# Performance work log

Measured on AMD Instinct MI355X. Metric: run time of the kernel, lower is better.

## Reference

```python
import jax, jax.numpy as jnp
import numpy as np

S1 = 2048      # seqx1_dim
S2 = 2048      # seqx2_dim
E1 = 1024      # seqx1_emb_dim
E2 = 1024      # seqx2_emb_dim
U = 1024       # units
M = E1 + E2    # margex_dim
B = 2048
TAU = 0.5


def setup_inputs() -> dict:
    key = jax.random.key(0)
    ks = jax.random.split(key, 20)
    g = lambda k, shp, fan: jax.random.normal(k, shp, jnp.float32) * (1.0 / np.sqrt(fan))
    bias = jnp.zeros((4 * U,), jnp.float32).at[U:2 * U].set(1.0)  # unit_forget_bias
    return {
        'inputs': jax.random.normal(ks[0], (B, S1 + S2), jnp.float32),
        'h_tm1': jax.random.normal(ks[1], (B, U), jnp.float32),
        'c_tm1': jax.random.normal(ks[2], (B, U), jnp.float32),
        'crohis_tm': jax.random.normal(ks[3], (B, M), jnp.float32),
        'embed_w1': g(ks[4], (S1, E1), S1),
        'embed_w2': g(ks[5], (S2, E2), S2),
        'w12_w': g(ks[6], (E1, E1), E1),
        'w12_u': g(ks[7], (E2, E1), E2),
        'w12_v': g(ks[8], (E2, E1), E2),
        'w21_w': g(ks[9], (E2, E2), E2),
        'w21_u': g(ks[10], (E1, E2), E1),
        'w21_v': g(ks[11], (E1, E2), E1),
        'crohis_w': g(ks[12], (M, U), M),
        'crohis_b': jnp.zeros((U,), jnp.float32),
        'decomp_w': g(ks[13], (M, M), M),
        'decomp_b': jnp.zeros((M,), jnp.float32),
        'kernel': g(ks[14], (M, 4 * U), M),
        'recurrent_kernel': g(ks[15], (U, 4 * U), U),
        'bias': bias,
    }


def _cell(inputs, h_tm1, c_tm1, crohis_tm, embed_w1, embed_w2, w12_w, w12_u, w12_v,
          w21_w, w21_u, w21_v, crohis_w, crohis_b, decomp_w, decomp_b,
          kernel, recurrent_kernel, bias):
    seqx1 = inputs[:, :S1]
    seqx2 = inputs[:, S1:]
    e1 = seqx1 @ embed_w1                                   # [B,E1]
    e2 = seqx2 @ embed_w2                                   # [B,E2]
    # dual cross-attention gates (softmax over feature axis, as K.softmax default)
    ca12 = jax.nn.softmax(jnp.tanh(e1 @ w12_w + e2 @ w12_u) * (e2 @ w12_v), axis=-1)
    ca21 = jax.nn.softmax(jnp.tanh(e2 @ w21_w + e1 @ w21_u) * (e1 @ w21_v), axis=-1)
    x = jnp.concatenate([e1 * ca12, e2 * ca21], axis=-1)    # [B,M]
    # cross-history decomposition gate and decayed merge
    decomp = jax.nn.sigmoid(crohis_tm @ decomp_w + decomp_b)
    crohis = TAU * crohis_tm * decomp + (1.0 - TAU) * x     # [B,M]
    h_cro = jnp.tanh(crohis @ crohis_w + crohis_b)          # [B,U]
    # fused LSTM (implementation=2)
    z = x @ kernel + h_tm1 @ recurrent_kernel + bias        # [B,4U]
    zi, zf, zc, zo = jnp.split(z, 4, axis=-1)
    i = jax.nn.sigmoid(zi)
    f = jax.nn.sigmoid(zf)
    c = f * c_tm1 + i * jnp.tanh(zc)
    o = jax.nn.sigmoid(zo)
    h = o * jnp.tanh(c) + h_cro
    return h, c, crohis


def reference(inputs, h_tm1, c_tm1, crohis_tm, embed_w1, embed_w2, w12_w, w12_u, w12_v,
              w21_w, w21_u, w21_v, crohis_w, crohis_b, decomp_w, decomp_b,
              kernel, recurrent_kernel, bias):
    return _cell(inputs, h_tm1, c_tm1, crohis_tm, embed_w1, embed_w2, w12_w, w12_u,
                 w12_v, w21_w, w21_u, w21_v, crohis_w, crohis_b, decomp_w, decomp_b,
                 kernel, recurrent_kernel, bias)
```

## Files before the change

### kernel.cpp

```cpp
#include <hip/hip_runtime.h>
#include <stdint.h>

typedef unsigned short u16;
typedef __bf16 bf16x8 __attribute__((ext_vector_type(8)));
typedef float f32x4 __attribute__((ext_vector_type(4)));
typedef u16 u16x8 __attribute__((ext_vector_type(8)));

__device__ __forceinline__ u16 bf16_bits(float f) {
  uint32_t x = __float_as_uint(f);
  uint32_t r = (x + 0x7FFFu + ((x >> 16) & 1u)) >> 16;
  return (u16)r;
}
__device__ __forceinline__ float bits_f32(u16 u) {
  return __uint_as_float(((uint32_t)u) << 16);
}
__device__ __forceinline__ float sigm(float x) { return 1.f / (1.f + expf(-x)); }

__device__ __forceinline__ void gload_lds16(const void* g, void* l) {
  __builtin_amdgcn_global_load_lds(
      (const __attribute__((address_space(1))) void*)g,
      (__attribute__((address_space(3))) void*)l,
      16, 0, 0);
}

__global__ __launch_bounds__(256) void cvt_all_kernel(
    const float* __restrict__ inp, const float* __restrict__ ctm,
    const float* __restrict__ h, u16* __restrict__ bf_in,
    u16* __restrict__ bf_ctm, u16* __restrict__ xh) {
  int i = blockIdx.x * 256 + threadIdx.x;
  const float* src;
  u16* dst;
  if (i < 1048576) {
    src = inp + (size_t)i * 8;
    dst = bf_in + (size_t)i * 8;
  } else if (i < 1048576 + 524288) {
    int j = i - 1048576;
    src = ctm + (size_t)j * 8;
    dst = bf_ctm + (size_t)j * 8;
  } else {
    int j = i - 1572864;
    int row = j >> 7;
    int c0 = (j & 127) << 3;
    src = h + (size_t)row * 1024 + c0;
    dst = xh + (size_t)row * 3072 + 2048 + c0;
  }
  const f32x4* s = (const f32x4*)src;
  f32x4 a = s[0], b = s[1];
  u16x8 o;
#pragma unroll
  for (int k = 0; k < 4; ++k) { o[k] = bf16_bits(a[k]); o[4 + k] = bf16_bits(b[k]); }
  *(u16x8*)dst = o;
}

struct TransGroups {
  const float* src[12];
  u16* dst[12];
  int N[12];
  int ld[12];
  long long off[12];
  int start[13];
};

__global__ __launch_bounds__(256) void transpose_all_kernel(TransGroups tg) {
  __shared__ float t[64][33];
  int bid = blockIdx.x;
  int g = 0;
#pragma unroll
  for (int i = 1; i < 12; ++i)
    if (bid >= tg.start[i]) g = i;
  int local = bid - tg.start[g];
  const float* src = tg.src[g];
  u16* dst = tg.dst[g];
  int N = tg.N[g];
  int ld = tg.ld[g];
  long long off = tg.off[g];
  int ntn = N >> 5;
  int n0 = (local % ntn) << 5;
  int k0 = (local / ntn) << 6;
  int tx = threadIdx.x & 31, ty = threadIdx.x >> 5;
#pragma unroll
  for (int r = ty; r < 64; r += 8) t[r][tx] = src[(size_t)(k0 + r) * N + n0 + tx];
  __syncthreads();
#pragma unroll
  for (int j = ty; j < 32; j += 8) {
    uint32_t lo = bf16_bits(t[2 * tx][j]);
    uint32_t hi = bf16_bits(t[2 * tx + 1][j]);
    *(uint32_t*)(&dst[off + (size_t)(n0 + j) * ld + k0 + 2 * tx]) = lo | (hi << 16);
  }
}

enum { EPI_F32 = 0, EPI_BF16 = 1, EPI_DHALF = 2, EPI_TANH = 3 };

struct GemmGroups {
  const u16* A[4];
  const u16* Bt[4];
  float* C[4];
  u16* Cb[4];
  const float* bias[4];
  const float* aux[4];
  int lda[4];
  int K[4];
  int nbx[4];
  int ldc[4];
  int ldcb[4];
  int epi[4];
  int start[4];
};

__global__ __launch_bounds__(256) void gemm_grouped(GemmGroups gg) {
  __shared__ u16 As[2][4096];
  __shared__ u16 Bs[2][4096];
  const int bid = blockIdx.x;
  int g = 0;
#pragma unroll
  for (int i = 1; i < 4; ++i)
    if (bid >= gg.start[i]) g = i;
  const int local = bid - gg.start[g];
  const u16* __restrict__ A = gg.A[g];
  const u16* __restrict__ Bt = gg.Bt[g];
  const int lda = gg.lda[g];
  const int K = gg.K[g];
  const int nbx = gg.nbx[g];

  const int tid = threadIdx.x;
  const int lane = tid & 63;
  const int wid = tid >> 6;
  const int wr = wid >> 1, wc = wid & 1;
  const int brow = (local / nbx) * 128;
  const int bcol = (local % nbx) * 128;

  f32x4 acc[4][4] = {};

  const int s0 = wid, s1 = wid + 4;
  const int oA0 = s0 * 1024 + lane * 16;
  const int oA1 = s1 * 1024 + lane * 16;

  const char* gA0 = (const char*)A + (((size_t)(brow + (oA0 >> 6)) * lda) << 1) + (oA0 & 63);
  const char* gA1 = (const char*)A + (((size_t)(brow + (oA1 >> 6)) * lda) << 1) + (oA1 & 63);
  const char* gB0 = (const char*)Bt + (((size_t)(bcol + (oA0 >> 6)) * K) << 1) + (oA0 & 63);
  const char* gB1 = (const char*)Bt + (((size_t)(bcol + (oA1 >> 6)) * K) << 1) + (oA1 & 63);

#define STAGE(buf, koff)                                              \
  {                                                                   \
    gload_lds16(gA0 + (koff), (char*)As + (buf) * 8192 + s0 * 1024);  \
    gload_lds16(gA1 + (koff), (char*)As + (buf) * 8192 + s1 * 1024);  \
    gload_lds16(gB0 + (koff), (char*)Bs + (buf) * 8192 + s0 * 1024);  \
    gload_lds16(gB1 + (koff), (char*)Bs + (buf) * 8192 + s1 * 1024);  \
  }

  const int nk = K >> 5;
  STAGE(0, 0);
  __syncthreads();
  int cur = 0;
  for (int kt = 0; kt < nk; ++kt) {
    const int koff = (kt + 1 < nk ? kt + 1 : kt) << 6;
    STAGE(cur ^ 1, koff);

    const char* Ab = (const char*)As + cur * 8192;
    const char* Bb = (const char*)Bs + cur * 8192;
    bf16x8 af[4], bfr[4];
#pragma unroll
    for (int m = 0; m < 4; ++m) {
      int r = wr * 64 + m * 16 + (lane & 15);
      af[m] = *(const bf16x8*)(Ab + r * 64 + ((lane >> 4) << 4));
    }
#pragma unroll
    for (int n = 0; n < 4; ++n) {
      int cidx = wc * 64 + n * 16 + (lane & 15);
      bfr[n] = *(const bf16x8*)(Bb + cidx * 64 + ((lane >> 4) << 4));
    }
#pragma unroll
    for (int m = 0; m < 4; ++m)
#pragma unroll
      for (int n = 0; n < 4; ++n)
        acc[m][n] = __builtin_amdgcn_mfma_f32_16x16x32_bf16(af[m], bfr[n], acc[m][n], 0, 0, 0);

    __syncthreads();
    cur ^= 1;
  }
#undef STAGE

  float* __restrict__ C = gg.C[g];
  u16* __restrict__ Cb = gg.Cb[g];
  const float* __restrict__ bias = gg.bias[g];
  const float* __restrict__ aux = gg.aux[g];
  const int ldc = gg.ldc[g];
  const int ldcb = gg.ldcb[g];
  const int epi = gg.epi[g];

  const int r0 = brow + wr * 64 + ((lane >> 4) << 2);
  const int c0 = bcol + wc * 64 + (lane & 15);
#pragma unroll
  for (int m = 0; m < 4; ++m) {
#pragma unroll
    for (int n = 0; n < 4; ++n) {
#pragma unroll
      for (int j = 0; j < 4; ++j) {
        int gr = r0 + m * 16 + j;
        int gc = c0 + n * 16;
        float v = acc[m][n][j];
        if (epi == EPI_F32) {
          C[(size_t)gr * ldc + gc] = v;
        } else if (epi == EPI_BF16) {
          Cb[(size_t)gr * ldcb + gc] = bf16_bits(v);
        } else if (epi == EPI_DHALF) {
          size_t ci = (size_t)gr * ldc + gc;
          C[ci] = 0.5f * aux[ci] * sigm(v + bias[gc]);
        } else {
          C[(size_t)gr * ldc + gc] = tanhf(v + bias[gc]);
        }
      }
    }
  }
}

__global__ __launch_bounds__(256) void softmax_cro_kernel(
    const float* __restrict__ T_ALL, const u16* __restrict__ E_B,
    const float* __restrict__ DCRO, u16* __restrict__ XH_B,
    float* __restrict__ out_cro, u16* __restrict__ CRO_B) {
  __shared__ float smx[4], sms[4];
  int row = blockIdx.x >> 1;
  int half = blockIdx.x & 1;
  const float* T = T_ALL + (size_t)row * 4096 + half * 1024;
  const float* V = T_ALL + (size_t)row * 4096 + 2048 + half * 1024;
  int tid = threadIdx.x;
  float s[4];
  float lmax = -1e30f;
#pragma unroll
  for (int i = 0; i < 4; ++i) {
    int c = tid + (i << 8);
    s[i] = tanhf(T[c]) * V[c];
    lmax = fmaxf(lmax, s[i]);
  }
#pragma unroll
  for (int o = 32; o; o >>= 1) lmax = fmaxf(lmax, __shfl_xor(lmax, o, 64));
  if ((tid & 63) == 0) smx[tid >> 6] = lmax;
  __syncthreads();
  float bmax = fmaxf(fmaxf(smx[0], smx[1]), fmaxf(smx[2], smx[3]));
  float lsum = 0.f;
#pragma unroll
  for (int i = 0; i < 4; ++i) { s[i] = expf(s[i] - bmax); lsum += s[i]; }
#pragma unroll
  for (int o = 32; o; o >>= 1) lsum += __shfl_xor(lsum, o, 64);
  if ((tid & 63) == 0) sms[tid >> 6] = lsum;
  __syncthreads();
  float inv = 1.f / (sms[0] + sms[1] + sms[2] + sms[3]);
#pragma unroll
  for (int i = 0; i < 4; ++i) {
    int c = tid + (i << 8);
    int col = half * 1024 + c;
    size_t mi = (size_t)row * 2048 + col;
    float x = bits_f32(E_B[mi]) * s[i] * inv;
    XH_B[(size_t)row * 3072 + col] = bf16_bits(x);
    float cro = DCRO[mi] + 0.5f * x;
    out_cro[mi] = cro;
    CRO_B[mi] = bf16_bits(cro);
  }
}

__global__ __launch_bounds__(256) void gates_kernel(
    const float* __restrict__ Z, const float* __restrict__ bias,
    const float* __restrict__ c_tm1, const float* __restrict__ hcro,
    float* __restrict__ out_h, float* __restrict__ out_c) {
  int i = blockIdx.x * 256 + threadIdx.x;
  int row = i >> 8;
  int u0 = (i & 255) << 2;
  const float* zr = Z + (size_t)row * 4096;
  f32x4 zi = *(const f32x4*)(zr + u0);
  f32x4 zf = *(const f32x4*)(zr + 1024 + u0);
  f32x4 zc = *(const f32x4*)(zr + 2048 + u0);
  f32x4 zo = *(const f32x4*)(zr + 3072 + u0);
  f32x4 bi = *(const f32x4*)(bias + u0);
  f32x4 bff = *(const f32x4*)(bias + 1024 + u0);
  f32x4 bc = *(const f32x4*)(bias + 2048 + u0);
  f32x4 bo = *(const f32x4*)(bias + 3072 + u0);
  f32x4 ct = *(const f32x4*)(c_tm1 + (size_t)row * 1024 + u0);
  f32x4 hc = *(const f32x4*)(hcro + (size_t)row * 1024 + u0);
  f32x4 h, c;
#pragma unroll
  for (int k = 0; k < 4; ++k) {
    float I = sigm(zi[k] + bi[k]);
    float F = sigm(zf[k] + bff[k]);
    float O = sigm(zo[k] + bo[k]);
    float cc = F * ct[k] + I * tanhf(zc[k] + bc[k]);
    c[k] = cc;
    h[k] = O * tanhf(cc) + hc[k];
  }
  *(f32x4*)(out_h + (size_t)row * 1024 + u0) = h;
  *(f32x4*)(out_c + (size_t)row * 1024 + u0) = c;
}

extern "C" void kernel_launch(void* const* d_in, const int* in_sizes, int n_in,
                              void* d_out, int out_size, void* d_ws, size_t ws_size,
                              hipStream_t stream) {
  const float* in_inputs = (const float*)d_in[0];
  const float* in_h      = (const float*)d_in[1];
  const float* in_c      = (const float*)d_in[2];
  const float* in_ctm    = (const float*)d_in[3];
  const float* w_e1      = (const float*)d_in[4];
  const float* w_e2      = (const float*)d_in[5];
  const float* w12w      = (const float*)d_in[6];
  const float* w12u      = (const float*)d_in[7];
  const float* w12v      = (const float*)d_in[8];
  const float* w21w      = (const float*)d_in[9];
  const float* w21u      = (const float*)d_in[10];
  const float* w21v      = (const float*)d_in[11];
  const float* w_cro     = (const float*)d_in[12];
  const float* b_cro     = (const float*)d_in[13];
  const float* w_dec     = (const float*)d_in[14];
  const float* b_dec     = (const float*)d_in[15];
  const float* w_k       = (const float*)d_in[16];
  const float* w_rk      = (const float*)d_in[17];
  const float* b_z       = (const float*)d_in[18];

  float* out_h   = (float*)d_out;
  float* out_c   = out_h + (size_t)2048 * 1024;
  float* out_cro = out_h + (size_t)2 * 2048 * 1024;

  char* ws = (char*)d_ws;
  size_t off = 0;
  auto alloc = [&](size_t bytes) {
    char* p = ws + off;
    off += (bytes + 255) & ~(size_t)255;
    return p;
  };
  u16* BF_IN    = (u16*)alloc((size_t)2048 * 4096 * 2);
  u16* BF_CROTM = (u16*)alloc((size_t)2048 * 2048 * 2);
  u16* E_B      = (u16*)alloc((size_t)2048 * 2048 * 2);
  float* T_ALL  = (float*)alloc((size_t)2048 * 4096 * 4);
  float* DCRO   = (float*)alloc((size_t)2048 * 2048 * 4);
  u16* XH_B     = (u16*)alloc((size_t)2048 * 3072 * 2);
  u16* CRO_B    = (u16*)alloc((size_t)2048 * 2048 * 2);
  float* HCRO   = (float*)alloc((size_t)2048 * 1024 * 4);
  u16* WT_E1    = (u16*)alloc((size_t)1024 * 2048 * 2);
  u16* WT_E2    = (u16*)alloc((size_t)1024 * 2048 * 2);
  u16* WT_T     = (u16*)alloc((size_t)2048 * 2048 * 2);
  u16* WT_V12   = (u16*)alloc((size_t)1024 * 1024 * 2);
  u16* WT_V21   = (u16*)alloc((size_t)1024 * 1024 * 2);
  u16* WT_CRO   = (u16*)alloc((size_t)1024 * 2048 * 2);
  u16* WT_DEC   = (u16*)alloc((size_t)2048 * 2048 * 2);
  u16* WT_KRK   = (u16*)alloc((size_t)4096 * 3072 * 2);
  float* Z = T_ALL;

  const int INF = 0x7fffffff;

  cvt_all_kernel<<<7168, 256, 0, stream>>>(in_inputs, in_ctm, in_h, BF_IN, BF_CROTM, XH_B);

  {
    TransGroups tg;
    int s = 0, gi = 0;
    auto add = [&](const float* src, int K, int N, u16* dst, int ld, long long dOff) {
      tg.src[gi] = src; tg.dst[gi] = dst; tg.N[gi] = N; tg.ld[gi] = ld; tg.off[gi] = dOff;
      tg.start[gi] = s; s += (K >> 6) * (N >> 5); ++gi;
    };
    add(w_e1, 2048, 1024, WT_E1, 2048, 0);
    add(w_e2, 2048, 1024, WT_E2, 2048, 0);
    add(w12w, 1024, 1024, WT_T, 2048, 0);
    add(w12u, 1024, 1024, WT_T, 2048, 1024);
    add(w21u, 1024, 1024, WT_T, 2048, (long long)1024 * 2048);
    add(w21w, 1024, 1024, WT_T, 2048, (long long)1024 * 2048 + 1024);
    add(w12v, 1024, 1024, WT_V12, 1024, 0);
    add(w21v, 1024, 1024, WT_V21, 1024, 0);
    add(w_cro, 2048, 1024, WT_CRO, 2048, 0);
    add(w_dec, 2048, 2048, WT_DEC, 2048, 0);
    add(w_k, 2048, 4096, WT_KRK, 3072, 0);
    add(w_rk, 1024, 4096, WT_KRK, 3072, 2048);
    tg.start[12] = s;
    transpose_all_kernel<<<s, 256, 0, stream>>>(tg);
  }

  auto mkgrp = [&]() {
    GemmGroups gg;
    for (int i = 0; i < 4; ++i) {
      gg.A[i] = nullptr; gg.Bt[i] = nullptr; gg.C[i] = nullptr; gg.Cb[i] = nullptr;
      gg.bias[i] = nullptr; gg.aux[i] = nullptr;
      gg.lda[i] = 0; gg.K[i] = 32; gg.nbx[i] = 1; gg.ldc[i] = 0; gg.ldcb[i] = 0;
      gg.epi[i] = EPI_F32; gg.start[i] = INF;
    }
    return gg;
  };

  {
    GemmGroups gg = mkgrp();
    gg.A[0] = BF_CROTM; gg.Bt[0] = WT_DEC; gg.lda[0] = 2048; gg.K[0] = 2048;
    gg.nbx[0] = 16; gg.C[0] = DCRO; gg.ldc[0] = 2048; gg.epi[0] = EPI_DHALF;
    gg.bias[0] = b_dec; gg.aux[0] = in_ctm; gg.start[0] = 0;
    gg.A[1] = BF_IN; gg.Bt[1] = WT_E1; gg.lda[1] = 4096; gg.K[1] = 2048;
    gg.nbx[1] = 8; gg.Cb[1] = E_B; gg.ldcb[1] = 2048; gg.epi[1] = EPI_BF16;
    gg.start[1] = 256;
    gg.A[2] = BF_IN + 2048; gg.Bt[2] = WT_E2; gg.lda[2] = 4096; gg.K[2] = 2048;
    gg.nbx[2] = 8; gg.Cb[2] = E_B + 1024; gg.ldcb[2] = 2048; gg.epi[2] = EPI_BF16;
    gg.start[2] = 384;
    gemm_grouped<<<512, 256, 0, stream>>>(gg);
  }

  {
    GemmGroups gg = mkgrp();
    gg.A[0] = E_B; gg.Bt[0] = WT_T; gg.lda[0] = 2048; gg.K[0] = 2048;
    gg.nbx[0] = 16; gg.C[0] = T_ALL; gg.ldc[0] = 4096; gg.epi[0] = EPI_F32;
    gg.start[0] = 0;
    gg.A[1] = E_B + 1024; gg.Bt[1] = WT_V12; gg.lda[1] = 2048; gg.K[1] = 1024;
    gg.nbx[1] = 8; gg.C[1] = T_ALL + 2048; gg.ldc[1] = 4096; gg.epi[1] = EPI_F32;
    gg.start[1] = 256;
    gg.A[2] = E_B; gg.Bt[2] = WT_V21; gg.lda[2] = 2048; gg.K[2] = 1024;
    gg.nbx[2] = 8; gg.C[2] = T_ALL + 3072; gg.ldc[2] = 4096; gg.epi[2] = EPI_F32;
    gg.start[2] = 384;
    gemm_grouped<<<512, 256, 0, stream>>>(gg);
  }

  softmax_cro_kernel<<<4096, 256, 0, stream>>>(T_ALL, E_B, DCRO, XH_B, out_cro, CRO_B);

  {
    GemmGroups gg = mkgrp();
    gg.A[0] = XH_B; gg.Bt[0] = WT_KRK; gg.lda[0] = 3072; gg.K[0] = 3072;
    gg.nbx[0] = 32; gg.C[0] = Z; gg.ldc[0] = 4096; gg.epi[0] = EPI_F32;
    gg.start[0] = 0;
    gg.A[1] = CRO_B; gg.Bt[1] = WT_CRO; gg.lda[1] = 2048; gg.K[1] = 2048;
    gg.nbx[1] = 8; gg.C[1] = HCRO; gg.ldc[1] = 1024; gg.epi[1] = EPI_TANH;
    gg.bias[1] = b_cro; gg.start[1] = 512;
    gemm_grouped<<<640, 256, 0, stream>>>(gg);
  }

  gates_kernel<<<2048, 256, 0, stream>>>(Z, b_z, in_c, HCRO, out_h, out_c);
}
```

Baseline: 497.8 us.

## Split-K GEMM groups to double block count and fold reductions into consumers

Adds a separate B leading dimension so each GEMM can be split along K into two groups writing partial sums. The two partials are combined in the softmax and gates kernels, which also take over the tanh epilogue for the cross-history projection. The V projections are now stored as bf16. The intent is to raise the number of blocks per launch (512→768, 640→1280) to fill the many CUs, at the cost of extra fp32 partial-sum traffic and reduced bf16 precision on V.

```diff
diff --git a/kernel.cpp b/kernel.cpp
--- a/kernel.cpp
+++ b/kernel.cpp
@@ -89,7 +89,7 @@
   }
 }
 
-enum { EPI_F32 = 0, EPI_BF16 = 1, EPI_DHALF = 2, EPI_TANH = 3 };
+enum { EPI_F32 = 0, EPI_BF16 = 1, EPI_DHALF = 2 };
 
 struct GemmGroups {
   const u16* A[4];
@@ -99,6 +99,7 @@
   const float* bias[4];
   const float* aux[4];
   int lda[4];
+  int ldb[4];
   int K[4];
   int nbx[4];
   int ldc[4];
@@ -119,6 +120,7 @@
   const u16* __restrict__ A = gg.A[g];
   const u16* __restrict__ Bt = gg.Bt[g];
   const int lda = gg.lda[g];
+  const int ldb = gg.ldb[g];
   const int K = gg.K[g];
   const int nbx = gg.nbx[g];
 
@@ -137,8 +139,8 @@
 
   const char* gA0 = (const char*)A + (((size_t)(brow + (oA0 >> 6)) * lda) << 1) + (oA0 & 63);
   const char* gA1 = (const char*)A + (((size_t)(brow + (oA1 >> 6)) * lda) << 1) + (oA1 & 63);
-  const char* gB0 = (const char*)Bt + (((size_t)(bcol + (oA0 >> 6)) * K) << 1) + (oA0 & 63);
-  const char* gB1 = (const char*)Bt + (((size_t)(bcol + (oA1 >> 6)) * K) << 1) + (oA1 & 63);
+  const char* gB0 = (const char*)Bt + (((size_t)(bcol + (oA0 >> 6)) * ldb) << 1) + (oA0 & 63);
+  const char* gB1 = (const char*)Bt + (((size_t)(bcol + (oA1 >> 6)) * ldb) << 1) + (oA1 & 63);
 
 #define STAGE(buf, koff)                                              \
   {                                                                   \
@@ -203,11 +205,9 @@
           C[(size_t)gr * ldc + gc] = v;
         } else if (epi == EPI_BF16) {
           Cb[(size_t)gr * ldcb + gc] = bf16_bits(v);
-        } else if (epi == EPI_DHALF) {
+        } else {
           size_t ci = (size_t)gr * ldc + gc;
           C[ci] = 0.5f * aux[ci] * sigm(v + bias[gc]);
-        } else {
-          C[(size_t)gr * ldc + gc] = tanhf(v + bias[gc]);
         }
       }
     }
@@ -215,21 +215,22 @@
 }
 
 __global__ __launch_bounds__(256) void softmax_cro_kernel(
-    const float* __restrict__ T_ALL, const u16* __restrict__ E_B,
-    const float* __restrict__ DCRO, u16* __restrict__ XH_B,
+    const float* __restrict__ TP0, const float* __restrict__ TP1,
+    const u16* __restrict__ TV_B, const float* __restrict__ DCRO,
+    const u16* __restrict__ E_B, u16* __restrict__ XH_B,
     float* __restrict__ out_cro, u16* __restrict__ CRO_B) {
   __shared__ float smx[4], sms[4];
   int row = blockIdx.x >> 1;
   int half = blockIdx.x & 1;
-  const float* T = T_ALL + (size_t)row * 4096 + half * 1024;
-  const float* V = T_ALL + (size_t)row * 4096 + 2048 + half * 1024;
+  size_t base = (size_t)row * 2048 + half * 1024;
   int tid = threadIdx.x;
   float s[4];
   float lmax = -1e30f;
 #pragma unroll
   for (int i = 0; i < 4; ++i) {
     int c = tid + (i << 8);
-    s[i] = tanhf(T[c]) * V[c];
+    float t = TP0[base + c] + TP1[base + c];
+    s[i] = tanhf(t) * bits_f32(TV_B[base + c]);
     lmax = fmaxf(lmax, s[i]);
   }
 #pragma unroll
@@ -259,32 +260,42 @@
 }
 
 __global__ __launch_bounds__(256) void gates_kernel(
-    const float* __restrict__ Z, const float* __restrict__ bias,
-    const float* __restrict__ c_tm1, const float* __restrict__ hcro,
-    float* __restrict__ out_h, float* __restrict__ out_c) {
+    const float* __restrict__ ZP0, const float* __restrict__ ZP1,
+    const float* __restrict__ bias, const float* __restrict__ c_tm1,
+    const float* __restrict__ HP0, const float* __restrict__ HP1,
+    const float* __restrict__ b_cro, float* __restrict__ out_h,
+    float* __restrict__ out_c) {
   int i = blockIdx.x * 256 + threadIdx.x;
   int row = i >> 8;
   int u0 = (i & 255) << 2;
-  const float* zr = Z + (size_t)row * 4096;
-  f32x4 zi = *(const f32x4*)(zr + u0);
-  f32x4 zf = *(const f32x4*)(zr + 1024 + u0);
-  f32x4 zc = *(const f32x4*)(zr + 2048 + u0);
-  f32x4 zo = *(const f32x4*)(zr + 3072 + u0);
+  size_t zb = (size_t)row * 4096;
+  f32x4 zi = *(const f32x4*)(ZP0 + zb + u0);
+  f32x4 zf = *(const f32x4*)(ZP0 + zb + 1024 + u0);
+  f32x4 zc = *(const f32x4*)(ZP0 + zb + 2048 + u0);
+  f32x4 zo = *(const f32x4*)(ZP0 + zb + 3072 + u0);
+  f32x4 yi = *(const f32x4*)(ZP1 + zb + u0);
+  f32x4 yf = *(const f32x4*)(ZP1 + zb + 1024 + u0);
+  f32x4 yc = *(const f32x4*)(ZP1 + zb + 2048 + u0);
+  f32x4 yo = *(const f32x4*)(ZP1 + zb + 3072 + u0);
   f32x4 bi = *(const f32x4*)(bias + u0);
   f32x4 bff = *(const f32x4*)(bias + 1024 + u0);
   f32x4 bc = *(const f32x4*)(bias + 2048 + u0);
   f32x4 bo = *(const f32x4*)(bias + 3072 + u0);
-  f32x4 ct = *(const f32x4*)(c_tm1 + (size_t)row * 1024 + u0);
-  f32x4 hc = *(const f32x4*)(hcro + (size_t)row * 1024 + u0);
+  size_t hb = (size_t)row * 1024 + u0;
+  f32x4 ct = *(const f32x4*)(c_tm1 + hb);
+  f32x4 h0 = *(const f32x4*)(HP0 + hb);
+  f32x4 h1 = *(const f32x4*)(HP1 + hb);
+  f32x4 bcr = *(const f32x4*)(b_cro + u0);
   f32x4 h, c;
 #pragma unroll
   for (int k = 0; k < 4; ++k) {
-    float I = sigm(zi[k] + bi[k]);
-    float F = sigm(zf[k] + bff[k]);
-    float O = sigm(zo[k] + bo[k]);
-    float cc = F * ct[k] + I * tanhf(zc[k] + bc[k]);
+    float I = sigm(zi[k] + yi[k] + bi[k]);
+    float F = sigm(zf[k] + yf[k] + bff[k]);
+    float O = sigm(zo[k] + yo[k] + bo[k]);
+    float cc = F * ct[k] + I * tanhf(zc[k] + yc[k] + bc[k]);
+    float hcro = tanhf(h0[k] + h1[k] + bcr[k]);
     c[k] = cc;
-    h[k] = O * tanhf(cc) + hc[k];
+    h[k] = O * tanhf(cc) + hcro;
   }
   *(f32x4*)(out_h + (size_t)row * 1024 + u0) = h;
   *(f32x4*)(out_c + (size_t)row * 1024 + u0) = c;
@@ -327,11 +338,8 @@
   u16* BF_IN    = (u16*)alloc((size_t)2048 * 4096 * 2);
   u16* BF_CROTM = (u16*)alloc((size_t)2048 * 2048 * 2);
   u16* E_B      = (u16*)alloc((size_t)2048 * 2048 * 2);
-  float* T_ALL  = (float*)alloc((size_t)2048 * 4096 * 4);
-  float* DCRO   = (float*)alloc((size_t)2048 * 2048 * 4);
   u16* XH_B     = (u16*)alloc((size_t)2048 * 3072 * 2);
   u16* CRO_B    = (u16*)alloc((size_t)2048 * 2048 * 2);
-  float* HCRO   = (float*)alloc((size_t)2048 * 1024 * 4);
   u16* WT_E1    = (u16*)alloc((size_t)1024 * 2048 * 2);
   u16* WT_E2    = (u16*)alloc((size_t)1024 * 2048 * 2);
   u16* WT_T     = (u16*)alloc((size_t)2048 * 2048 * 2);
@@ -340,9 +348,14 @@
   u16* WT_CRO   = (u16*)alloc((size_t)1024 * 2048 * 2);
   u16* WT_DEC   = (u16*)alloc((size_t)2048 * 2048 * 2);
   u16* WT_KRK   = (u16*)alloc((size_t)4096 * 3072 * 2);
-  float* Z = T_ALL;
-
-  const int INF = 0x7fffffff;
+  float* TP0    = (float*)alloc((size_t)2048 * 2048 * 4);
+  float* TP1    = (float*)alloc((size_t)2048 * 2048 * 4);
+  u16* TV_B     = (u16*)alloc((size_t)2048 * 2048 * 2);
+  float* DCRO   = (float*)alloc((size_t)2048 * 2048 * 4);
+  float* ZP0 = (float*)ws;
+  float* ZP1 = TP0;
+  float* HP0 = (float*)TV_B;
+  float* HP1 = DCRO;
 
   cvt_all_kernel<<<7168, 256, 0, stream>>>(in_inputs, in_ctm, in_h, BF_IN, BF_CROTM, XH_B);
 
@@ -374,52 +387,63 @@
     for (int i = 0; i < 4; ++i) {
       gg.A[i] = nullptr; gg.Bt[i] = nullptr; gg.C[i] = nullptr; gg.Cb[i] = nullptr;
       gg.bias[i] = nullptr; gg.aux[i] = nullptr;
-      gg.lda[i] = 0; gg.K[i] = 32; gg.nbx[i] = 1; gg.ldc[i] = 0; gg.ldcb[i] = 0;
-      gg.epi[i] = EPI_F32; gg.start[i] = INF;
+      gg.lda[i] = 0; gg.ldb[i] = 32; gg.K[i] = 32; gg.nbx[i] = 1;
+      gg.ldc[i] = 0; gg.ldcb[i] = 0; gg.epi[i] = EPI_F32; gg.start[i] = 0x7fffffff;
     }
     return gg;
   };
 
   {
     GemmGroups gg = mkgrp();
-    gg.A[0] = BF_CROTM; gg.Bt[0] = WT_DEC; gg.lda[0] = 2048; gg.K[0] = 2048;
-    gg.nbx[0] = 16; gg.C[0] = DCRO; gg.ldc[0] = 2048; gg.epi[0] = EPI_DHALF;
-    gg.bias[0] = b_dec; gg.aux[0] = in_ctm; gg.start[0] = 0;
-    gg.A[1] = BF_IN; gg.Bt[1] = WT_E1; gg.lda[1] = 4096; gg.K[1] = 2048;
-    gg.nbx[1] = 8; gg.Cb[1] = E_B; gg.ldcb[1] = 2048; gg.epi[1] = EPI_BF16;
-    gg.start[1] = 256;
-    gg.A[2] = BF_IN + 2048; gg.Bt[2] = WT_E2; gg.lda[2] = 4096; gg.K[2] = 2048;
-    gg.nbx[2] = 8; gg.Cb[2] = E_B + 1024; gg.ldcb[2] = 2048; gg.epi[2] = EPI_BF16;
-    gg.start[2] = 384;
+    gg.A[0] = BF_CROTM; gg.Bt[0] = WT_DEC; gg.lda[0] = 2048; gg.ldb[0] = 2048;
+    gg.K[0] = 2048; gg.nbx[0] = 16; gg.C[0] = DCRO; gg.ldc[0] = 2048;
+    gg.epi[0] = EPI_DHALF; gg.bias[0] = b_dec; gg.aux[0] = in_ctm; gg.start[0] = 0;
+    gg.A[1] = BF_IN; gg.Bt[1] = WT_E1; gg.lda[1] = 4096; gg.ldb[1] = 2048;
+    gg.K[1] = 2048; gg.nbx[1] = 8; gg.Cb[1] = E_B; gg.ldcb[1] = 2048;
+    gg.epi[1] = EPI_BF16; gg.start[1] = 256;
+    gg.A[2] = BF_IN + 2048; gg.Bt[2] = WT_E2; gg.lda[2] = 4096; gg.ldb[2] = 2048;
+    gg.K[2] = 2048; gg.nbx[2] = 8; gg.Cb[2] = E_B + 1024; gg.ldcb[2] = 2048;
+    gg.epi[2] = EPI_BF16; gg.start[2] = 384;
     gemm_grouped<<<512, 256, 0, stream>>>(gg);
   }
 
   {
     GemmGroups gg = mkgrp();
-    gg.A[0] = E_B; gg.Bt[0] = WT_T; gg.lda[0] = 2048; gg.K[0] = 2048;
-    gg.nbx[0] = 16; gg.C[0] = T_ALL; gg.ldc[0] = 4096; gg.epi[0] = EPI_F32;
-    gg.start[0] = 0;
-    gg.A[1] = E_B + 1024; gg.Bt[1] = WT_V12; gg.lda[1] = 2048; gg.K[1] = 1024;
-    gg.nbx[1] = 8; gg.C[1] = T_ALL + 2048; gg.ldc[1] = 4096; gg.epi[1] = EPI_F32;
-    gg.start[1] = 256;
-    gg.A[2] = E_B; gg.Bt[2] = WT_V21; gg.lda[2] = 2048; gg.K[2] = 1024;
-    gg.nbx[2] = 8; gg.C[2] = T_ALL + 3072; gg.ldc[2] = 4096; gg.epi[2] = EPI_F32;
-    gg.start[2] = 384;
-    gemm_grouped<<<512, 256, 0, stream>>>(gg);
-  }
-
-  softmax_cro_kernel<<<4096, 256, 0, stream>>>(T_ALL, E_B, DCRO, XH_B, out_cro, CRO_B);
+    gg.A[0] = E_B; gg.Bt[0] = WT_T; gg.lda[0] = 2048; gg.ldb[0] = 2048;
+    gg.K[0] = 1024; gg.nbx[0] = 16; gg.C[0] = TP0; gg.ldc[0] = 2048;
+    gg.epi[0] = EPI_F32; gg.start[0] = 0;
+    gg.A[1] = E_B + 1024; gg.Bt[1] = WT_T + 1024; gg.lda[1] = 2048; gg.ldb[1] = 2048;
+    gg.K[1] = 1024; gg.nbx[1] = 16; gg.C[1] = TP1; gg.ldc[1] = 2048;
+    gg.epi[1] = EPI_F32; gg.start[1] = 256;
+    gg.A[2] = E_B + 1024; gg.Bt[2] = WT_V12; gg.lda[2] = 2048; gg.ldb[2] = 1024;
+    gg.K[2] = 1024; gg.nbx[2] = 8; gg.Cb[2] = TV_B; gg.ldcb[2] = 2048;
+    gg.epi[2] = EPI_BF16; gg.start[2] = 512;
+    gg.A[3] = E_B; gg.Bt[3] = WT_V21; gg.lda[3] = 2048; gg.ldb[3] = 1024;
+    gg.K[3] = 1024; gg.nbx[3] = 8; gg.Cb[3] = TV_B + 1024; gg.ldcb[3] = 2048;
+    gg.epi[3] = EPI_BF16; gg.start[3] = 640;
+    gemm_grouped<<<768, 256, 0, stream>>>(gg);
+  }
+
+  softmax_cro_kernel<<<4096, 256, 0, stream>>>(TP0, TP1, TV_B, DCRO, E_B,
+                                               XH_B, out_cro, CRO_B);
 
   {
     GemmGroups gg = mkgrp();
-    gg.A[0] = XH_B; gg.Bt[0] = WT_KRK; gg.lda[0] = 3072; gg.K[0] = 3072;
-    gg.nbx[0] = 32; gg.C[0] = Z; gg.ldc[0] = 4096; gg.epi[0] = EPI_F32;
-    gg.start[0] = 0;
-    gg.A[1] = CRO_B; gg.Bt[1] = WT_CRO; gg.lda[1] = 2048; gg.K[1] = 2048;
-    gg.nbx[1] = 8; gg.C[1] = HCRO; gg.ldc[1] = 1024; gg.epi[1] = EPI_TANH;
-    gg.bias[1] = b_cro; gg.start[1] = 512;
-    gemm_grouped<<<640, 256, 0, stream>>>(gg);
-  }
-
-  gates_kernel<<<2048, 256, 0, stream>>>(Z, b_z, in_c, HCRO, out_h, out_c);
-}
+    gg.A[0] = XH_B; gg.Bt[0] = WT_KRK; gg.lda[0] = 3072; gg.ldb[0] = 3072;
+    gg.K[0] = 1536; gg.nbx[0] = 32; gg.C[0] = ZP0; gg.ldc[0] = 4096;
+    gg.epi[0] = EPI_F32; gg.start[0] = 0;
+    gg.A[1] = XH_B + 1536; gg.Bt[1] = WT_KRK + 1536; gg.lda[1] = 3072; gg.ldb[1] = 3072;
+    gg.K[1] = 1536; gg.nbx[1] = 32; gg.C[1] = ZP1; gg.ldc[1] = 4096;
+    gg.epi[1] = EPI_F32; gg.start[1] = 512;
+    gg.A[2] = CRO_B; gg.Bt[2] = WT_CRO; gg.lda[2] = 2048; gg.ldb[2] = 2048;
+    gg.K[2] = 1024; gg.nbx[2] = 8; gg.C[2] = HP0; gg.ldc[2] = 1024;
+    gg.epi[2] = EPI_F32; gg.start[2] = 1024;
+    gg.A[3] = CRO_B + 1024; gg.Bt[3] = WT_CRO + 1024; gg.lda[3] = 2048; gg.ldb[3] = 2048;
+    gg.K[3] = 1024; gg.nbx[3] = 8; gg.C[3] = HP1; gg.ldc[3] = 1024;
+    gg.epi[3] = EPI_F32; gg.start[3] = 1152;
+    gemm_grouped<<<1280, 256, 0, stream>>>(gg);
+  }
+
+  gates_kernel<<<2048, 256, 0, stream>>>(ZP0, ZP1, b_z, in_c, HP0, HP1, b_cro,
+                                         out_h, out_c);
+}
```

Result: no change. 490.3 us (-1.5%).
